# Performance work log

Hardware: AMD Instinct MI355X
Metric: run time of the kernel (lower is better)

Reference implementation:

```python
import jax, jax.numpy as jnp
import numpy as np

D_MODEL = 256
N_HEADS = 8
N_LEVELS = 4
NUM_POINTS_LIST = [4, 4, 4, 4]
SUM_POINTS = sum(NUM_POINTS_LIST)
TOTAL_POINTS = N_HEADS * SUM_POINTS
HEAD_DIM = D_MODEL // N_HEADS
OFFSET_SCALE = 0.5
SPATIAL_SHAPES = np.array([[80, 80], [40, 40], [20, 20], [10, 10]], dtype=np.int64)


def setup_inputs() -> dict:
    key = jax.random.key(0)
    ks = jax.random.split(key, 7)
    B, NQ = 16, 300
    seq = int((SPATIAL_SHAPES[:, 0] * SPATIAL_SHAPES[:, 1]).sum())  # 8500
    s = 1.0 / np.sqrt(D_MODEL)
    return {
        'hidden_states': jax.random.normal(ks[0], (B, NQ, D_MODEL), jnp.float32),
        'encoder_hidden_states': jax.random.normal(ks[1], (B, seq, D_MODEL), jnp.float32),
        'reference_points': jax.random.uniform(ks[2], (B, NQ, 1, 4), jnp.float32, 0.05, 0.95),
        'spatial_shapes': SPATIAL_SHAPES,
        'w_off': jax.random.uniform(ks[3], (TOTAL_POINTS * 2, D_MODEL), jnp.float32, -s, s),
        'b_off': jax.random.uniform(ks[4], (TOTAL_POINTS * 2,), jnp.float32, -s, s),
        'w_attn': jax.random.uniform(ks[5], (TOTAL_POINTS, D_MODEL), jnp.float32, -s, s),
        'b_attn': jax.random.uniform(ks[6], (TOTAL_POINTS,), jnp.float32, -s, s),
    }


def _grid_sample_zeros(img_flat, H, W, gx, gy):
    # img_flat: [N, H*W, C]; gx, gy: [N, Q, P] unnormalized pixel coords.
    # Bilinear, padding_mode='zeros', align_corners=False semantics of torch.grid_sample.
    x0 = jnp.floor(gx)
    y0 = jnp.floor(gy)
    wx = (gx - x0)[..., None]
    wy = (gy - y0)[..., None]
    x0i = x0.astype(jnp.int32)
    y0i = y0.astype(jnp.int32)

    def gather(xi, yi):
        valid = (xi >= 0) & (xi < W) & (yi >= 0) & (yi < H)
        idx = jnp.clip(yi, 0, H - 1) * W + jnp.clip(xi, 0, W - 1)
        N = img_flat.shape[0]
        v = jnp.take_along_axis(img_flat, idx.reshape(N, -1)[..., None], axis=1)
        v = v.reshape(idx.shape + (img_flat.shape[-1],))
        return v * valid[..., None]

    v00 = gather(x0i, y0i)
    v01 = gather(x0i + 1, y0i)
    v10 = gather(x0i, y0i + 1)
    v11 = gather(x0i + 1, y0i + 1)
    top = v00 * (1 - wx) + v01 * wx
    bot = v10 * (1 - wx) + v11 * wx
    return top * (1 - wy) + bot * wy  # [N, Q, P, C]


def reference(hidden_states, encoder_hidden_states, reference_points, spatial_shapes, w_off, b_off, w_attn, b_attn):
    B, NQ, _ = hidden_states.shape
    seq = encoder_hidden_states.shape[1]
    shapes = np.asarray(spatial_shapes)

    value = encoder_hidden_states.reshape(B, seq, N_HEADS, HEAD_DIM)

    off = (hidden_states @ w_off.T + b_off).reshape(B, NQ, N_HEADS, SUM_POINTS, 2)
    attn = jax.nn.softmax((hidden_states @ w_attn.T + b_attn).reshape(B, NQ, N_HEADS, SUM_POINTS), axis=-1)

    # reference_points: [B, NQ, 1, 4] (cx, cy, w, h) in [0,1]
    nps = jnp.asarray(np.repeat([1.0 / n for n in NUM_POINTS_LIST], NUM_POINTS_LIST), hidden_states.dtype)[:, None]
    offset = off * nps * reference_points[:, :, None, :, 2:] * OFFSET_SCALE
    sampling_locations = reference_points[:, :, None, :, :2] + offset  # [B,NQ,H,P,2]

    grids = 2.0 * sampling_locations - 1.0
    value_bh = value.transpose(0, 2, 1, 3).reshape(B * N_HEADS, seq, HEAD_DIM)
    grids_bh = grids.transpose(0, 2, 1, 3, 4).reshape(B * N_HEADS, NQ, SUM_POINTS, 2)

    outs = []
    start_s, start_p = 0, 0
    for lvl in range(N_LEVELS):
        Hl, Wl = int(shapes[lvl, 0]), int(shapes[lvl, 1])
        Pl = NUM_POINTS_LIST[lvl]
        img = value_bh[:, start_s:start_s + Hl * Wl]  # [BH, Hl*Wl, hd]
        g = grids_bh[:, :, start_p:start_p + Pl]
        gx = (g[..., 0] + 1.0) * Wl / 2.0 - 0.5
        gy = (g[..., 1] + 1.0) * Hl / 2.0 - 0.5
        outs.append(_grid_sample_zeros(img, Hl, Wl, gx, gy))
        start_s += Hl * Wl
        start_p += Pl

    sampled = jnp.concatenate(outs, axis=2)  # [BH, NQ, SUM_POINTS, hd]
    attn_bh = attn.transpose(0, 2, 1, 3).reshape(B * N_HEADS, NQ, SUM_POINTS, 1)
    out = (sampled * attn_bh).sum(axis=2)  # [BH, NQ, hd]
    out = out.reshape(B, N_HEADS, NQ, HEAD_DIM).transpose(0, 2, 1, 3).reshape(B, NQ, D_MODEL)
    return (out, attn)
```

## Files before the change

### kernel.cpp

```cpp
#include <hip/hip_runtime.h>
#include <hip/hip_bf16.h>

#define BQ_TOTAL 4800
#define D_MODEL 256
#define N_HEADS 8
#define SUM_POINTS 16
#define HEAD_DIM 32
#define SEQ 8500
#define OUT_ELEMS (BQ_TOTAL * D_MODEL)

typedef _Float16 half8 __attribute__((ext_vector_type(8)));
typedef _Float16 half4 __attribute__((ext_vector_type(4)));
typedef float floatx4 __attribute__((ext_vector_type(4)));

#define LDK 264

__global__ __launch_bounds__(256) void gemm_logits_mfma(
    const float* __restrict__ hs,
    const float* __restrict__ w_off, const float* __restrict__ b_off,
    const float* __restrict__ w_attn, const float* __restrict__ b_attn,
    float* __restrict__ off_out, float* __restrict__ attn_out)
{
    __shared__ _Float16 Asld[64 * LDK];
    __shared__ _Float16 Bsld[64 * LDK];

    const int tid = threadIdx.x;
    const int row0 = blockIdx.x * 64;
    const int col0 = blockIdx.y * 64;

    const float* Bsrc; const float* bias;
    if (col0 < 256) { Bsrc = w_off  + (size_t)col0 * 256;        bias = b_off  + col0; }
    else            { Bsrc = w_attn + (size_t)(col0 - 256) * 256; bias = b_attn + (col0 - 256); }

    #pragma unroll
    for (int i = 0; i < 16; i++) {
        const int idx = tid + i * 256;
        const int r = idx >> 6;
        const int kc = (idx & 63) << 2;

        const float4 a = *(const float4*)(hs + (size_t)(row0 + r) * 256 + kc);
        half4 ah; ah[0] = (_Float16)a.x; ah[1] = (_Float16)a.y;
                  ah[2] = (_Float16)a.z; ah[3] = (_Float16)a.w;
        *(half4*)&Asld[r * LDK + kc] = ah;

        const float4 b = *(const float4*)(Bsrc + (size_t)r * 256 + kc);
        half4 bh; bh[0] = (_Float16)b.x; bh[1] = (_Float16)b.y;
                  bh[2] = (_Float16)b.z; bh[3] = (_Float16)b.w;
        *(half4*)&Bsld[r * LDK + kc] = bh;
    }
    __syncthreads();

    const int wv = tid >> 6;
    const int lane = tid & 63;
    const int m = lane & 15;
    const int quad = lane >> 4;

    half8 af[8];
    #pragma unroll
    for (int q8 = 0; q8 < 8; q8++)
        af[q8] = *(const half8*)&Asld[(wv * 16 + m) * LDK + q8 * 32 + quad * 8];

    floatx4 acc[4] = {{0.f,0.f,0.f,0.f},{0.f,0.f,0.f,0.f},{0.f,0.f,0.f,0.f},{0.f,0.f,0.f,0.f}};
    #pragma unroll
    for (int ct = 0; ct < 4; ct++) {
        #pragma unroll
        for (int q8 = 0; q8 < 8; q8++) {
            const half8 bf = *(const half8*)&Bsld[(ct * 16 + m) * LDK + q8 * 32 + quad * 8];
            acc[ct] = __builtin_amdgcn_mfma_f32_16x16x32_f16(af[q8], bf, acc[ct], 0, 0, 0);
        }
    }

    #pragma unroll
    for (int ct = 0; ct < 4; ct++) {
        const int col_l = ct * 16 + m;
        const float bv = bias[col_l];
        #pragma unroll
        for (int rg = 0; rg < 4; rg++) {
            const int row = row0 + wv * 16 + quad * 4 + rg;
            const float v = acc[ct][rg] + bv;
            if (col0 < 256)
                off_out[(size_t)row * 256 + col0 + col_l] = v;
            else
                attn_out[(size_t)row * 128 + (col0 - 256) + col_l] = v;
        }
    }
}

__global__ __launch_bounds__(256) void deform_sample(
    const float* __restrict__ enc,
    const float* __restrict__ refp,
    const float* __restrict__ offlog,
    float* __restrict__ attn,
    float* __restrict__ out)
{
    const int tid = threadIdx.x;
    const int w = tid >> 6;
    const int lane = tid & 63;

    const int orig = blockIdx.x;
    const int bswz = (orig & 7) * 1200 + (orig >> 3);

    const int item = bswz * 4 + w;
    const int bq = item >> 3;
    const int h = item & 7;
    const int p = lane >> 2;
    const int sub = lane & 3;

    float* attn_ptr = attn + (size_t)bq * 128 + h * 16;
    const float l = attn_ptr[p];
    const float2 off2 = *(const float2*)(offlog + (size_t)bq * 256 + h * 32 + 2 * p);
    const float4 rp4 = *(const float4*)(refp + (size_t)bq * 4);

    const int lvl = p >> 2;
    const int Wl = 80 >> lvl;
    int base = 0;
    if (lvl == 1) base = 6400;
    else if (lvl == 2) base = 8000;
    else if (lvl == 3) base = 8400;

    const float Wf = (float)Wl;
    const float gx = (rp4.x + off2.x * 0.125f * rp4.z) * Wf - 0.5f;
    const float gy = (rp4.y + off2.y * 0.125f * rp4.w) * Wf - 0.5f;
    const float x0f = floorf(gx), y0f = floorf(gy);
    const float fx = gx - x0f, fy = gy - y0f;
    const int x0 = (int)x0f, y0 = (int)y0f;

    const int b = bq / 300;
    const float* pbase = enc + ((size_t)b * SEQ + base) * 256 + h * 32 + sub * 4;

    float4 va[4], vb[4];
    float wgt[4];
    #pragma unroll
    for (int c = 0; c < 4; c++) {
        const int xc = x0 + (c & 1);
        const int yc = y0 + (c >> 1);
        const float wx = (c & 1) ? fx : (1.0f - fx);
        const float wy = (c >> 1) ? fy : (1.0f - fy);
        const bool valid = (xc >= 0) && (xc < Wl) && (yc >= 0) && (yc < Wl);
        const int xi = min(max(xc, 0), Wl - 1);
        const int yi = min(max(yc, 0), Wl - 1);
        wgt[c] = valid ? wx * wy : 0.0f;
        const float* vp = pbase + (size_t)(yi * Wl + xi) * 256;
        va[c] = *(const float4*)(vp);
        vb[c] = *(const float4*)(vp + 16);
    }

    float m = l;
    #pragma unroll
    for (int s = 4; s < 64; s <<= 1) m = fmaxf(m, __shfl_xor(m, s));
    const float e = __expf(l - m);
    float ssum = e;
    #pragma unroll
    for (int s = 4; s < 64; s <<= 1) ssum += __shfl_xor(ssum, s);
    const float prob = e / ssum;
    if (sub == 0) attn_ptr[p] = prob;

    float4 acc0 = {0.f, 0.f, 0.f, 0.f};
    float4 acc1 = {0.f, 0.f, 0.f, 0.f};
    #pragma unroll
    for (int c = 0; c < 4; c++) {
        acc0.x += wgt[c] * va[c].x; acc0.y += wgt[c] * va[c].y;
        acc0.z += wgt[c] * va[c].z; acc0.w += wgt[c] * va[c].w;
        acc1.x += wgt[c] * vb[c].x; acc1.y += wgt[c] * vb[c].y;
        acc1.z += wgt[c] * vb[c].z; acc1.w += wgt[c] * vb[c].w;
    }

    float vals[8];
    vals[0] = acc0.x * prob; vals[1] = acc0.y * prob;
    vals[2] = acc0.z * prob; vals[3] = acc0.w * prob;
    vals[4] = acc1.x * prob; vals[5] = acc1.y * prob;
    vals[6] = acc1.z * prob; vals[7] = acc1.w * prob;

    float red[4];
    #pragma unroll
    for (int i = 0; i < 4; i++) {
        const float send = (lane & 32) ? vals[i] : vals[i + 4];
        const float recv = __shfl_xor(send, 32);
        red[i] = ((lane & 32) ? vals[i + 4] : vals[i]) + recv;
    }
    #pragma unroll
    for (int s = 4; s < 32; s <<= 1) {
        #pragma unroll
        for (int i = 0; i < 4; i++) red[i] += __shfl_xor(red[i], s);
    }

    if ((lane & 28) == 0) {
        float4 v; v.x = red[0]; v.y = red[1]; v.z = red[2]; v.w = red[3];
        *(float4*)(out + (size_t)bq * 256 + h * 32 + ((lane >> 5) << 4) + (sub << 2)) = v;
    }
}

extern "C" void kernel_launch(void* const* d_in, const int* in_sizes, int n_in,
                              void* d_out, int out_size, void* d_ws, size_t ws_size,
                              hipStream_t stream) {
    const float* hs     = (const float*)d_in[0];
    const float* enc    = (const float*)d_in[1];
    const float* refp   = (const float*)d_in[2];
    const float* w_off  = (const float*)d_in[4];
    const float* b_off  = (const float*)d_in[5];
    const float* w_attn = (const float*)d_in[6];
    const float* b_attn = (const float*)d_in[7];

    float* out  = (float*)d_out;
    float* attn = out + OUT_ELEMS;
    float* offlog = (float*)d_ws;

    dim3 g1(BQ_TOTAL / 64, 384 / 64);
    gemm_logits_mfma<<<g1, 256, 0, stream>>>(hs, w_off, b_off, w_attn, b_attn, offlog, attn);

    deform_sample<<<(BQ_TOTAL * N_HEADS) / 4, 256, 0, stream>>>(enc, refp, offlog, attn, out);
}
```

Measured before the change: 219.4 us.

## Split point preprocessing into a separate kernel writing indices and weights

Moves the softmax, sampling-coordinate and bilinear-weight computation into a new prep_points kernel, with one thread per point. That kernel writes int4 corner indices and float4 weights, folded with the attention probability, to workspace buffers. The sampling kernel then only loads these and gathers, which removes the four-times-redundant per-lane arithmetic and softmax shuffles from it. In exchange it adds a kernel launch and a global round trip of about 9.8 MB for the index and weight buffers.

Result: no change. 223.1 us (+1.7%).

```diff
diff --git a/kernel.cpp b/kernel.cpp
--- a/kernel.cpp
+++ b/kernel.cpp
@@ -8,6 +8,7 @@
 #define HEAD_DIM 32
 #define SEQ 8500
 #define OUT_ELEMS (BQ_TOTAL * D_MODEL)
+#define NPTS_TOTAL (BQ_TOTAL * N_HEADS * SUM_POINTS)
 
 typedef _Float16 half8 __attribute__((ext_vector_type(8)));
 typedef _Float16 half4 __attribute__((ext_vector_type(4)));
@@ -86,30 +87,31 @@
     }
 }
 
-__global__ __launch_bounds__(256) void deform_sample(
-    const float* __restrict__ enc,
+__global__ __launch_bounds__(256) void prep_points(
     const float* __restrict__ refp,
     const float* __restrict__ offlog,
     float* __restrict__ attn,
-    float* __restrict__ out)
+    int4* __restrict__ idx_buf,
+    float4* __restrict__ w_buf)
 {
-    const int tid = threadIdx.x;
-    const int w = tid >> 6;
-    const int lane = tid & 63;
-
-    const int orig = blockIdx.x;
-    const int bswz = (orig & 7) * 1200 + (orig >> 3);
-
-    const int item = bswz * 4 + w;
-    const int bq = item >> 3;
-    const int h = item & 7;
-    const int p = lane >> 2;
-    const int sub = lane & 3;
-
-    float* attn_ptr = attn + (size_t)bq * 128 + h * 16;
-    const float l = attn_ptr[p];
+    const int g = blockIdx.x * 256 + threadIdx.x;
+    const int p = g & 15;
+    const int h = (g >> 4) & 7;
+    const int bq = g >> 7;
+
+    const float l = attn[g];
     const float2 off2 = *(const float2*)(offlog + (size_t)bq * 256 + h * 32 + 2 * p);
     const float4 rp4 = *(const float4*)(refp + (size_t)bq * 4);
+
+    float m = l;
+    #pragma unroll
+    for (int s = 1; s < 16; s <<= 1) m = fmaxf(m, __shfl_xor(m, s));
+    const float e = __expf(l - m);
+    float ssum = e;
+    #pragma unroll
+    for (int s = 1; s < 16; s <<= 1) ssum += __shfl_xor(ssum, s);
+    const float prob = e / ssum;
+    attn[g] = prob;
 
     const int lvl = p >> 2;
     const int Wl = 80 >> lvl;
@@ -125,11 +127,8 @@
     const float fx = gx - x0f, fy = gy - y0f;
     const int x0 = (int)x0f, y0 = (int)y0f;
 
-    const int b = bq / 300;
-    const float* pbase = enc + ((size_t)b * SEQ + base) * 256 + h * 32 + sub * 4;
-
-    float4 va[4], vb[4];
-    float wgt[4];
+    int   ii[4];
+    float ww[4];
     #pragma unroll
     for (int c = 0; c < 4; c++) {
         const int xc = x0 + (c & 1);
@@ -139,37 +138,55 @@
         const bool valid = (xc >= 0) && (xc < Wl) && (yc >= 0) && (yc < Wl);
         const int xi = min(max(xc, 0), Wl - 1);
         const int yi = min(max(yc, 0), Wl - 1);
-        wgt[c] = valid ? wx * wy : 0.0f;
-        const float* vp = pbase + (size_t)(yi * Wl + xi) * 256;
-        va[c] = *(const float4*)(vp);
-        vb[c] = *(const float4*)(vp + 16);
-    }
-
-    float m = l;
-    #pragma unroll
-    for (int s = 4; s < 64; s <<= 1) m = fmaxf(m, __shfl_xor(m, s));
-    const float e = __expf(l - m);
-    float ssum = e;
-    #pragma unroll
-    for (int s = 4; s < 64; s <<= 1) ssum += __shfl_xor(ssum, s);
-    const float prob = e / ssum;
-    if (sub == 0) attn_ptr[p] = prob;
-
-    float4 acc0 = {0.f, 0.f, 0.f, 0.f};
-    float4 acc1 = {0.f, 0.f, 0.f, 0.f};
+        ii[c] = base + yi * Wl + xi;
+        ww[c] = valid ? wx * wy * prob : 0.0f;
+    }
+    int4 iv; iv.x = ii[0]; iv.y = ii[1]; iv.z = ii[2]; iv.w = ii[3];
+    float4 wv; wv.x = ww[0]; wv.y = ww[1]; wv.z = ww[2]; wv.w = ww[3];
+    idx_buf[g] = iv;
+    w_buf[g] = wv;
+}
+
+__global__ __launch_bounds__(256) void deform_sample(
+    const float* __restrict__ enc,
+    const int4* __restrict__ idx_buf,
+    const float4* __restrict__ w_buf,
+    float* __restrict__ out)
+{
+    const int tid = threadIdx.x;
+    const int w = tid >> 6;
+    const int lane = tid & 63;
+
+    const int orig = blockIdx.x;
+    const int bswz = (orig & 7) * 1200 + (orig >> 3);
+
+    const int item = bswz * 4 + w;
+    const int bq = item >> 3;
+    const int h = item & 7;
+    const int p = lane >> 2;
+    const int sub = lane & 3;
+
+    const int g = (item << 4) | p;
+    const int4 iv = idx_buf[g];
+    const float4 wv = w_buf[g];
+
+    const int b = bq / 300;
+    const float* pbase = enc + ((size_t)b * SEQ) * 256 + h * 32 + sub * 4;
+
+    float vals[8] = {0.f,0.f,0.f,0.f,0.f,0.f,0.f,0.f};
+    const int  idx4[4] = {iv.x, iv.y, iv.z, iv.w};
+    const float wgt4[4] = {wv.x, wv.y, wv.z, wv.w};
     #pragma unroll
     for (int c = 0; c < 4; c++) {
-        acc0.x += wgt[c] * va[c].x; acc0.y += wgt[c] * va[c].y;
-        acc0.z += wgt[c] * va[c].z; acc0.w += wgt[c] * va[c].w;
-        acc1.x += wgt[c] * vb[c].x; acc1.y += wgt[c] * vb[c].y;
-        acc1.z += wgt[c] * vb[c].z; acc1.w += wgt[c] * vb[c].w;
-    }
-
-    float vals[8];
-    vals[0] = acc0.x * prob; vals[1] = acc0.y * prob;
-    vals[2] = acc0.z * prob; vals[3] = acc0.w * prob;
-    vals[4] = acc1.x * prob; vals[5] = acc1.y * prob;
-    vals[6] = acc1.z * prob; vals[7] = acc1.w * prob;
+        const float* vp = pbase + ((size_t)idx4[c] << 8);
+        const float4 va = *(const float4*)(vp);
+        const float4 vb = *(const float4*)(vp + 16);
+        const float wgt = wgt4[c];
+        vals[0] += wgt * va.x; vals[1] += wgt * va.y;
+        vals[2] += wgt * va.z; vals[3] += wgt * va.w;
+        vals[4] += wgt * vb.x; vals[5] += wgt * vb.y;
+        vals[6] += wgt * vb.z; vals[7] += wgt * vb.w;
+    }
 
     float red[4];
     #pragma unroll
@@ -203,10 +220,15 @@
 
     float* out  = (float*)d_out;
     float* attn = out + OUT_ELEMS;
+
     float* offlog = (float*)d_ws;
+    int4*  idx_buf = (int4*)((char*)d_ws + (size_t)BQ_TOTAL * 256 * 4);
+    float4* w_buf  = (float4*)((char*)idx_buf + (size_t)NPTS_TOTAL * 16);
 
     dim3 g1(BQ_TOTAL / 64, 384 / 64);
     gemm_logits_mfma<<<g1, 256, 0, stream>>>(hs, w_off, b_off, w_attn, b_attn, offlog, attn);
 
-    deform_sample<<<(BQ_TOTAL * N_HEADS) / 4, 256, 0, stream>>>(enc, refp, offlog, attn, out);
-}
+    prep_points<<<NPTS_TOTAL / 256, 256, 0, stream>>>(refp, offlog, attn, idx_buf, w_buf);
+
+    deform_sample<<<(BQ_TOTAL * N_HEADS) / 4, 256, 0, stream>>>(enc, idx_buf, w_buf, out);
+}
```
